# Kernel optimization log

Measured on AMD Instinct MI355X. Metric: run time of the kernel, lower is better.

## Reference

```python
import jax, jax.numpy as jnp
import numpy as np

B, S, D_IN, D_OUT, H = 2, 2048, 1024, 1024, 16
HD = D_OUT // H


def setup_inputs() -> dict:
    key = jax.random.key(0)
    ks = jax.random.split(key, 6)
    s = 0.02
    return {
        "X": jax.random.normal(ks[0], (B, S, D_IN), dtype=jnp.float32),
        "Wq": jax.random.normal(ks[1], (D_OUT, D_IN), dtype=jnp.float32) * s,
        "Wk": jax.random.normal(ks[2], (D_OUT, D_IN), dtype=jnp.float32) * s,
        "Wv": jax.random.normal(ks[3], (D_OUT, D_IN), dtype=jnp.float32) * s,
        "Wo": jax.random.normal(ks[4], (D_OUT, D_OUT), dtype=jnp.float32) * s,
        "bo": jax.random.normal(ks[5], (D_OUT,), dtype=jnp.float32) * s,
    }


def reference(X, Wq, Wk, Wv, Wo, bo):
    b, n, _ = X.shape
    # torch Linear: y = x @ W^T
    Q = (X @ Wq.T).reshape(b, n, H, HD).transpose(0, 2, 1, 3)  # [b,h,s,hd]
    K = (X @ Wk.T).reshape(b, n, H, HD).transpose(0, 2, 1, 3)
    V = (X @ Wv.T).reshape(b, n, H, HD).transpose(0, 2, 1, 3)
    S_ = jnp.einsum('bhqd,bhkd->bhqk', Q, K)  # [b,h,s,s]
    causal = jnp.triu(jnp.ones((n, n), dtype=bool), k=1)
    S_ = jnp.where(causal, -jnp.inf, S_)
    W = jax.nn.softmax(S_ / jnp.sqrt(jnp.float32(HD)), axis=-1)
    Z = jnp.einsum('bhqk,bhkd->bhqd', W, V)
    Z = Z.transpose(0, 2, 1, 3).reshape(b, n, D_OUT)
    return Z @ Wo.T + bo
```

## Files before the change

### kernel.cpp

```cpp
#include <hip/hip_runtime.h>
#include <stdint.h>

typedef __bf16 bf16x8 __attribute__((ext_vector_type(8)));
typedef float  f32x4  __attribute__((ext_vector_type(4)));

#define S_   2048
#define DM   1024
#define QSCALE 0.18033688011112042f

__device__ __forceinline__ unsigned short f2b(float f) {
    uint32_t u = __builtin_bit_cast(uint32_t, f);
    u += 0x7fffu + ((u >> 16) & 1u);
    return (unsigned short)(u >> 16);
}

__device__ __forceinline__ uint32_t pack2bf(float a, float b) {
    uint32_t ua = __builtin_bit_cast(uint32_t, a) + 0x8000u;
    uint32_t ub = __builtin_bit_cast(uint32_t, b) + 0x8000u;
    return __builtin_amdgcn_perm(ub, ua, 0x07060302);
}

__device__ __forceinline__ void glds16(const void* g, void* l) {
    __builtin_amdgcn_global_load_lds(
        (const __attribute__((address_space(1))) void*)g,
        (__attribute__((address_space(3))) void*)l, 16, 0, 0);
}

__global__ void cvt_all(const float* __restrict__ X,
                        const float* __restrict__ Wq, const float* __restrict__ Wk,
                        const float* __restrict__ Wv,
                        unsigned short* __restrict__ Xb, unsigned short* __restrict__ Wb)
{
    size_t i = ((size_t)blockIdx.x * 256 + threadIdx.x) * 4;
    const float* src;
    unsigned short* dst;
    size_t off;
    if (i < (size_t)4194304) { src = X; dst = Xb; off = i; }
    else {
        size_t j = i - 4194304;
        int sel = (int)(j >> 20);
        off = j & 1048575;
        src = (sel == 0) ? Wq : (sel == 1) ? Wk : Wv;
        dst = Wb + (size_t)sel * 1048576;
    }
    float4 v = *(const float4*)&src[off];
    uint2 o;
    o.x = pack2bf(v.x, v.y);
    o.y = pack2bf(v.z, v.w);
    *(uint2*)&dst[off] = o;
}

__global__ __launch_bounds__(256, 2)
void qkv_gemm(const unsigned short* __restrict__ Xb,
              const unsigned short* __restrict__ Wqb,
              const unsigned short* __restrict__ Wkb,
              const unsigned short* __restrict__ Wvb,
              unsigned short* __restrict__ Qo, unsigned short* __restrict__ Ko,
              unsigned short* __restrict__ Vto)
{
    __shared__ unsigned short Ash[128 * 32];
    __shared__ unsigned short Bsh[128 * 32];

    const int t = threadIdx.x;
    const int lane = t & 63, w = t >> 6;
    const int lcol = lane & 15, quad = lane >> 4;
    const int z = blockIdx.z;
    const int rowBase = ((z == 2) ? blockIdx.x : blockIdx.y) * 128;
    const int colBase = ((z == 2) ? blockIdx.y : blockIdx.x) * 128;
    const unsigned short* aPtr = (z == 2) ? Wvb : Xb;
    const unsigned short* bPtr = (z == 0) ? Wqb : (z == 1) ? Wkb : Xb;
    const int wr = (w >> 1) * 64, wc = (w & 1) * 64;

    f32x4 acc[4][4];
    #pragma unroll
    for (int i = 0; i < 4; ++i)
        #pragma unroll
        for (int j = 0; j < 4; ++j) acc[i][j] = (f32x4){0.f,0.f,0.f,0.f};

    for (int k0 = 0; k0 < DM; k0 += 32) {
        __syncthreads();
        #pragma unroll
        for (int p = 0; p < 2; ++p) {
            int ci = p * 256 + t;
            glds16(&aPtr[(size_t)(rowBase + (ci >> 2)) * DM + k0 + (ci & 3) * 8], &Ash[ci * 8]);
        }
        #pragma unroll
        for (int p = 0; p < 2; ++p) {
            int ci = p * 256 + t;
            glds16(&bPtr[(size_t)(colBase + (ci >> 2)) * DM + k0 + (ci & 3) * 8], &Bsh[ci * 8]);
        }
        __syncthreads();
        bf16x8 af[4], bfr[4];
        #pragma unroll
        for (int i = 0; i < 4; ++i) af[i]  = *(const bf16x8*)&Ash[(wr + i*16 + lcol)*32 + quad*8];
        #pragma unroll
        for (int i = 0; i < 4; ++i) bfr[i] = *(const bf16x8*)&Bsh[(wc + i*16 + lcol)*32 + quad*8];
        #pragma unroll
        for (int i = 0; i < 4; ++i)
            #pragma unroll
            for (int j = 0; j < 4; ++j)
                acc[i][j] = __builtin_amdgcn_mfma_f32_16x16x32_bf16(af[i], bfr[j], acc[i][j], 0, 0, 0);
    }

    unsigned short* Cm = (z == 0) ? Qo : (z == 1) ? Ko : Vto;
    const int ld = (z == 2) ? (S_ * 2) : DM;
    const float sc = (z == 0) ? QSCALE : 1.0f;
    #pragma unroll
    for (int i = 0; i < 4; ++i)
        #pragma unroll
        for (int j = 0; j < 4; ++j)
            #pragma unroll
            for (int r = 0; r < 4; ++r) {
                int row = rowBase + wr + i*16 + quad*4 + r;
                int col = colBase + wc + j*16 + lcol;
                Cm[(size_t)row * ld + col] = f2b(acc[i][j][r] * sc);
            }
}

__global__ __launch_bounds__(512, 4)
void attn_kernel(const unsigned short* __restrict__ Q,
                 const unsigned short* __restrict__ K,
                 const unsigned short* __restrict__ Vt,
                 unsigned short* __restrict__ Z)
{
    __shared__ unsigned short Ks[128 * 72];
    __shared__ unsigned short Vts[64 * 136];
    __shared__ unsigned short Ps[128 * 136];

    const int t = threadIdx.x;
    const int lane = t & 63, w = t >> 6;
    const int lcol = lane & 15, quad = lane >> 4;

    const int bh = blockIdx.y;
    const int b = bh >> 4, h = bh & 15;
    const int tile = (bh < 16) ? (15 - (int)blockIdx.x) : (int)blockIdx.x;
    const int q0 = tile * 128;
    const int nchunk = tile + 1;

    const unsigned short* Qg = Q + (size_t)(b * S_ + q0) * DM + h * 64;
    const unsigned short* Kg = K + (size_t)(b * S_) * DM + h * 64;
    const unsigned short* Vg = Vt + (size_t)(h * 64) * (S_ * 2) + b * S_;

    bf16x8 qf[2];
    #pragma unroll
    for (int kd = 0; kd < 2; ++kd)
        qf[kd] = *(const bf16x8*)&Qg[(size_t)(w*16 + lcol) * DM + kd*32 + quad*8];

    bool mk[4];
    #pragma unroll
    for (int r = 0; r < 4; ++r) mk[r] = (quad*4 + r) > lcol;

    float lpart = 0.f;
    f32x4 o[4];
    #pragma unroll
    for (int nd = 0; nd < 4; ++nd) o[nd] = (f32x4){0.f,0.f,0.f,0.f};

    for (int c = 0; c < nchunk; ++c) {
        const int kc = c * 128;
        __syncthreads();
        #pragma unroll
        for (int p = 0; p < 2; ++p) {
            int ci = p * 512 + t;
            *(uint4*)&Ks[(ci >> 3) * 72 + (ci & 7) * 8] =
                *(const uint4*)&Kg[(size_t)(kc + (ci >> 3)) * DM + (ci & 7) * 8];
        }
        #pragma unroll
        for (int p = 0; p < 2; ++p) {
            int ci = p * 512 + t;
            *(uint4*)&Vts[(ci >> 4) * 136 + (ci & 15) * 8] =
                *(const uint4*)&Vg[(size_t)(ci >> 4) * (S_ * 2) + kc + (ci & 15) * 8];
        }
        __syncthreads();

        const bool diag = (c == nchunk - 1);
        const int nkmax = diag ? (w + 1) : 8;
        const int kdmax = diag ? ((w >> 1) + 1) : 4;

        #pragma unroll
        for (int nk = 0; nk < 8; ++nk) {
            if (nk < nkmax) {
                f32x4 s = (f32x4){0.f,0.f,0.f,0.f};
                bf16x8 ak0 = *(const bf16x8*)&Ks[(nk*16 + lcol)*72 + quad*8];
                s = __builtin_amdgcn_mfma_f32_16x16x32_bf16(ak0, qf[0], s, 0, 0, 0);
                bf16x8 ak1 = *(const bf16x8*)&Ks[(nk*16 + lcol)*72 + 32 + quad*8];
                s = __builtin_amdgcn_mfma_f32_16x16x32_bf16(ak1, qf[1], s, 0, 0, 0);
                float p0 = __builtin_amdgcn_exp2f(s[0]);
                float p1 = __builtin_amdgcn_exp2f(s[1]);
                float p2 = __builtin_amdgcn_exp2f(s[2]);
                float p3 = __builtin_amdgcn_exp2f(s[3]);
                if (diag && nk == w) {
                    p0 = mk[0] ? 0.f : p0;
                    p1 = mk[1] ? 0.f : p1;
                    p2 = mk[2] ? 0.f : p2;
                    p3 = mk[3] ? 0.f : p3;
                }
                lpart += (p0 + p1) + (p2 + p3);
                uint2 pk;
                pk.x = pack2bf(p0, p1);
                pk.y = pack2bf(p2, p3);
                *(uint2*)&Ps[(w*16 + lcol) * 136 + nk*16 + quad*4] = pk;
            } else if (nk < 2*kdmax) {
                *(uint2*)&Ps[(w*16 + lcol) * 136 + nk*16 + quad*4] = (uint2){0u, 0u};
            }
        }

        #pragma unroll
        for (int kd2 = 0; kd2 < 4; ++kd2) {
            if (kd2 < kdmax) {
                bf16x8 ap = *(const bf16x8*)&Ps[(w*16 + lcol) * 136 + kd2*32 + quad*8];
                #pragma unroll
                for (int nd = 0; nd < 4; ++nd) {
                    bf16x8 bv = *(const bf16x8*)&Vts[(nd*16 + lcol) * 136 + kd2*32 + quad*8];
                    o[nd] = __builtin_amdgcn_mfma_f32_16x16x32_bf16(ap, bv, o[nd], 0, 0, 0);
                }
            }
        }
    }

    lpart += __shfl_xor(lpart, 16);
    lpart += __shfl_xor(lpart, 32);
    float linv = 1.0f / lpart;
    #pragma unroll
    for (int r = 0; r < 4; ++r) {
        float lr = __shfl(linv, quad*4 + r);
        unsigned short* Zr = Z + (size_t)(b*S_ + q0 + w*16 + quad*4 + r) * DM + h*64;
        #pragma unroll
        for (int nd = 0; nd < 4; ++nd)
            Zr[nd*16 + lcol] = f2b(o[nd][r] * lr);
    }
}

__global__ __launch_bounds__(512, 2)
void out_gemm(const unsigned short* __restrict__ A,
              const float* __restrict__ Wo, const float* __restrict__ bo,
              float* __restrict__ Out)
{
    __shared__ unsigned short Ash[128 * 32];
    __shared__ unsigned short Bsh[128 * 32];

    const int t = threadIdx.x;
    const int lane = t & 63, w = t >> 6;
    const int lcol = lane & 15, quad = lane >> 4;
    const int rowBase = blockIdx.y * 128;
    const int colBase = blockIdx.x * 128;
    const int wr = (w >> 2) * 64, wc = (w & 3) * 32;

    f32x4 acc[4][2];
    #pragma unroll
    for (int i = 0; i < 4; ++i)
        #pragma unroll
        for (int j = 0; j < 2; ++j) acc[i][j] = (f32x4){0.f,0.f,0.f,0.f};

    for (int k0 = 0; k0 < DM; k0 += 32) {
        __syncthreads();
        glds16(&A[(size_t)(rowBase + (t >> 2)) * DM + k0 + (t & 3) * 8], &Ash[t * 8]);
        {
            const float* sb = Wo + (size_t)(colBase + (t >> 2)) * DM + k0 + (t & 3) * 8;
            float4 v0 = ((const float4*)sb)[0];
            float4 v1 = ((const float4*)sb)[1];
            uint4 tb;
            tb.x = pack2bf(v0.x, v0.y);
            tb.y = pack2bf(v0.z, v0.w);
            tb.z = pack2bf(v1.x, v1.y);
            tb.w = pack2bf(v1.z, v1.w);
            *(uint4*)&Bsh[(t >> 2) * 32 + (t & 3) * 8] = tb;
        }
        __syncthreads();
        bf16x8 af[4], bfr[2];
        #pragma unroll
        for (int i = 0; i < 4; ++i) af[i]  = *(const bf16x8*)&Ash[(wr + i*16 + lcol)*32 + quad*8];
        #pragma unroll
        for (int j = 0; j < 2; ++j) bfr[j] = *(const bf16x8*)&Bsh[(wc + j*16 + lcol)*32 + quad*8];
        #pragma unroll
        for (int i = 0; i < 4; ++i)
            #pragma unroll
            for (int j = 0; j < 2; ++j)
                acc[i][j] = __builtin_amdgcn_mfma_f32_16x16x32_bf16(af[i], bfr[j], acc[i][j], 0, 0, 0);
    }

    float bb[2];
    #pragma unroll
    for (int j = 0; j < 2; ++j) bb[j] = bo[colBase + wc + j*16 + lcol];

    #pragma unroll
    for (int i = 0; i < 4; ++i)
        #pragma unroll
        for (int j = 0; j < 2; ++j)
            #pragma unroll
            for (int r = 0; r < 4; ++r) {
                int row = rowBase + wr + i*16 + quad*4 + r;
                int col = colBase + wc + j*16 + lcol;
                Out[(size_t)row * DM + col] = acc[i][j][r] + bb[j];
            }
}

extern "C" void kernel_launch(void* const* d_in, const int* in_sizes, int n_in,
                              void* d_out, int out_size, void* d_ws, size_t ws_size,
                              hipStream_t stream) {
    const float* X  = (const float*)d_in[0];
    const float* Wq = (const float*)d_in[1];
    const float* Wk = (const float*)d_in[2];
    const float* Wv = (const float*)d_in[3];
    const float* Wo = (const float*)d_in[4];
    const float* bo = (const float*)d_in[5];
    float* out = (float*)d_out;

    unsigned short* Xb  = (unsigned short*)d_ws;
    unsigned short* Qw  = Xb + (size_t)4096 * 1024;
    unsigned short* Kw  = Qw + (size_t)4096 * 1024;
    unsigned short* Vtw = Kw + (size_t)4096 * 1024;
    unsigned short* Zb  = Xb;
    unsigned short* Wb  = (unsigned short*)d_out;

    cvt_all<<<dim3(7168), 256, 0, stream>>>(X, Wq, Wk, Wv, Xb, Wb);
    qkv_gemm<<<dim3(8, 32, 3), 256, 0, stream>>>(Xb, Wb, Wb + (size_t)1048576,
                                                 Wb + (size_t)2097152, Qw, Kw, Vtw);
    attn_kernel<<<dim3(16, 32), 512, 0, stream>>>(Qw, Kw, Vtw, Zb);
    out_gemm<<<dim3(8, 32), 512, 0, stream>>>(Zb, Wo, bo, out);
}
```

Measured before the change: 198.2 us.

## Prefetch K/V into registers, remap attention grid per XCD, pre-convert Wo to bf16

```diff
diff --git a/kernel.cpp b/kernel.cpp
--- a/kernel.cpp
+++ b/kernel.cpp
@@ -50,6 +50,16 @@
     *(uint2*)&dst[off] = o;
 }
 
+__global__ void cvt_wo(const float* __restrict__ Wo, unsigned short* __restrict__ Wob)
+{
+    size_t i = ((size_t)blockIdx.x * 256 + threadIdx.x) * 4;
+    float4 v = *(const float4*)&Wo[i];
+    uint2 o;
+    o.x = pack2bf(v.x, v.y);
+    o.y = pack2bf(v.z, v.w);
+    *(uint2*)&Wob[i] = o;
+}
+
 __global__ __launch_bounds__(256, 2)
 void qkv_gemm(const unsigned short* __restrict__ Xb,
               const unsigned short* __restrict__ Wqb,
@@ -131,9 +141,12 @@
     const int lane = t & 63, w = t >> 6;
     const int lcol = lane & 15, quad = lane >> 4;
 
-    const int bh = blockIdx.y;
+    const int g = blockIdx.x;
+    const int xcd = g & 7, slot = g >> 3;
+    const int bh = xcd * 4 + (slot & 3);
+    const int raw = slot >> 2;
+    const int tile = (raw < 8) ? (15 - 2 * raw) : (2 * (raw - 8));
     const int b = bh >> 4, h = bh & 15;
-    const int tile = (bh < 16) ? (15 - (int)blockIdx.x) : (int)blockIdx.x;
     const int q0 = tile * 128;
     const int nchunk = tile + 1;
 
@@ -155,20 +168,27 @@
     #pragma unroll
     for (int nd = 0; nd < 4; ++nd) o[nd] = (f32x4){0.f,0.f,0.f,0.f};
 
+    const int kr = t >> 3, kch = t & 7;
+    const int vr = t >> 4, vch = t & 15;
+
+    uint4 kreg[2], vreg[2];
+    kreg[0] = *(const uint4*)&Kg[(size_t)(kr)      * DM + kch * 8];
+    kreg[1] = *(const uint4*)&Kg[(size_t)(64 + kr) * DM + kch * 8];
+    vreg[0] = *(const uint4*)&Vg[(size_t)(vr)      * (S_ * 2) + vch * 8];
+    vreg[1] = *(const uint4*)&Vg[(size_t)(32 + vr) * (S_ * 2) + vch * 8];
+
     for (int c = 0; c < nchunk; ++c) {
-        const int kc = c * 128;
-        __syncthreads();
-        #pragma unroll
-        for (int p = 0; p < 2; ++p) {
-            int ci = p * 512 + t;
-            *(uint4*)&Ks[(ci >> 3) * 72 + (ci & 7) * 8] =
-                *(const uint4*)&Kg[(size_t)(kc + (ci >> 3)) * DM + (ci & 7) * 8];
-        }
-        #pragma unroll
-        for (int p = 0; p < 2; ++p) {
-            int ci = p * 512 + t;
-            *(uint4*)&Vts[(ci >> 4) * 136 + (ci & 15) * 8] =
-                *(const uint4*)&Vg[(size_t)(ci >> 4) * (S_ * 2) + kc + (ci & 15) * 8];
+        __syncthreads();
+        *(uint4*)&Ks[(kr)      * 72 + kch * 8] = kreg[0];
+        *(uint4*)&Ks[(64 + kr) * 72 + kch * 8] = kreg[1];
+        *(uint4*)&Vts[(vr)      * 136 + vch * 8] = vreg[0];
+        *(uint4*)&Vts[(32 + vr) * 136 + vch * 8] = vreg[1];
+        if (c + 1 < nchunk) {
+            const int kn = (c + 1) * 128;
+            kreg[0] = *(const uint4*)&Kg[(size_t)(kn + kr)      * DM + kch * 8];
+            kreg[1] = *(const uint4*)&Kg[(size_t)(kn + 64 + kr) * DM + kch * 8];
+            vreg[0] = *(const uint4*)&Vg[(size_t)(vr)      * (S_ * 2) + kn + vch * 8];
+            vreg[1] = *(const uint4*)&Vg[(size_t)(32 + vr) * (S_ * 2) + kn + vch * 8];
         }
         __syncthreads();
 
@@ -232,7 +252,7 @@
 
 __global__ __launch_bounds__(512, 2)
 void out_gemm(const unsigned short* __restrict__ A,
-              const float* __restrict__ Wo, const float* __restrict__ bo,
+              const unsigned short* __restrict__ Wob, const float* __restrict__ bo,
               float* __restrict__ Out)
 {
     __shared__ unsigned short Ash[128 * 32];
@@ -254,17 +274,7 @@
     for (int k0 = 0; k0 < DM; k0 += 32) {
         __syncthreads();
         glds16(&A[(size_t)(rowBase + (t >> 2)) * DM + k0 + (t & 3) * 8], &Ash[t * 8]);
-        {
-            const float* sb = Wo + (size_t)(colBase + (t >> 2)) * DM + k0 + (t & 3) * 8;
-            float4 v0 = ((const float4*)sb)[0];
-            float4 v1 = ((const float4*)sb)[1];
-            uint4 tb;
-            tb.x = pack2bf(v0.x, v0.y);
-            tb.y = pack2bf(v0.z, v0.w);
-            tb.z = pack2bf(v1.x, v1.y);
-            tb.w = pack2bf(v1.z, v1.w);
-            *(uint4*)&Bsh[(t >> 2) * 32 + (t & 3) * 8] = tb;
-        }
+        glds16(&Wob[(size_t)(colBase + (t >> 2)) * DM + k0 + (t & 3) * 8], &Bsh[t * 8]);
         __syncthreads();
         bf16x8 af[4], bfr[2];
         #pragma unroll
@@ -310,11 +320,13 @@
     unsigned short* Kw  = Qw + (size_t)4096 * 1024;
     unsigned short* Vtw = Kw + (size_t)4096 * 1024;
     unsigned short* Zb  = Xb;
+    unsigned short* Wob = Qw;
     unsigned short* Wb  = (unsigned short*)d_out;
 
     cvt_all<<<dim3(7168), 256, 0, stream>>>(X, Wq, Wk, Wv, Xb, Wb);
     qkv_gemm<<<dim3(8, 32, 3), 256, 0, stream>>>(Xb, Wb, Wb + (size_t)1048576,
                                                  Wb + (size_t)2097152, Qw, Kw, Vtw);
-    attn_kernel<<<dim3(16, 32), 512, 0, stream>>>(Qw, Kw, Vtw, Zb);
-    out_gemm<<<dim3(8, 32), 512, 0, stream>>>(Zb, Wo, bo, out);
-}
+    attn_kernel<<<dim3(512), 512, 0, stream>>>(Qw, Kw, Vtw, Zb);
+    cvt_wo<<<dim3(1024), 256, 0, stream>>>(Wo, Wob);
+    out_gemm<<<dim3(8, 32), 512, 0, stream>>>(Zb, Wob, bo, out);
+}
```

Result: slower. 205.2 us (+3.5%).

## Give each attention wave two query subtiles and pre-convert Wo to bf16

Applied to the files above, without the earlier changes.

```diff
diff --git a/kernel.cpp b/kernel.cpp
--- a/kernel.cpp
+++ b/kernel.cpp
@@ -50,6 +50,16 @@
     *(uint2*)&dst[off] = o;
 }
 
+__global__ void cvt_wo(const float* __restrict__ Wo, unsigned short* __restrict__ Wob)
+{
+    size_t i = ((size_t)blockIdx.x * 256 + threadIdx.x) * 4;
+    float4 v = *(const float4*)&Wo[i];
+    uint2 o;
+    o.x = pack2bf(v.x, v.y);
+    o.y = pack2bf(v.z, v.w);
+    *(uint2*)&Wob[i] = o;
+}
+
 __global__ __launch_bounds__(256, 2)
 void qkv_gemm(const unsigned short* __restrict__ Xb,
               const unsigned short* __restrict__ Wqb,
@@ -117,7 +127,7 @@
             }
 }
 
-__global__ __launch_bounds__(512, 4)
+__global__ __launch_bounds__(256, 2)
 void attn_kernel(const unsigned short* __restrict__ Q,
                  const unsigned short* __restrict__ K,
                  const unsigned short* __restrict__ Vt,
@@ -131,9 +141,10 @@
     const int lane = t & 63, w = t >> 6;
     const int lcol = lane & 15, quad = lane >> 4;
 
-    const int bh = blockIdx.y;
+    const int bh = blockIdx.x;
     const int b = bh >> 4, h = bh & 15;
-    const int tile = (bh < 16) ? (15 - (int)blockIdx.x) : (int)blockIdx.x;
+    const int y = blockIdx.y;
+    const int tile = (y < 8) ? (15 - y) : (y - 8);
     const int q0 = tile * 128;
     const int nchunk = tile + 1;
 
@@ -141,98 +152,131 @@
     const unsigned short* Kg = K + (size_t)(b * S_) * DM + h * 64;
     const unsigned short* Vg = Vt + (size_t)(h * 64) * (S_ * 2) + b * S_;
 
-    bf16x8 qf[2];
-    #pragma unroll
-    for (int kd = 0; kd < 2; ++kd)
-        qf[kd] = *(const bf16x8*)&Qg[(size_t)(w*16 + lcol) * DM + kd*32 + quad*8];
+    bf16x8 qf[2][2];
+    #pragma unroll
+    for (int qs = 0; qs < 2; ++qs)
+        #pragma unroll
+        for (int kd = 0; kd < 2; ++kd)
+            qf[qs][kd] = *(const bf16x8*)&Qg[(size_t)(w*32 + qs*16 + lcol) * DM + kd*32 + quad*8];
 
     bool mk[4];
     #pragma unroll
     for (int r = 0; r < 4; ++r) mk[r] = (quad*4 + r) > lcol;
 
-    float lpart = 0.f;
-    f32x4 o[4];
-    #pragma unroll
-    for (int nd = 0; nd < 4; ++nd) o[nd] = (f32x4){0.f,0.f,0.f,0.f};
+    float lpart[2] = {0.f, 0.f};
+    f32x4 o[2][4];
+    #pragma unroll
+    for (int qs = 0; qs < 2; ++qs)
+        #pragma unroll
+        for (int nd = 0; nd < 4; ++nd) o[qs][nd] = (f32x4){0.f,0.f,0.f,0.f};
 
     for (int c = 0; c < nchunk; ++c) {
         const int kc = c * 128;
         __syncthreads();
         #pragma unroll
-        for (int p = 0; p < 2; ++p) {
-            int ci = p * 512 + t;
+        for (int p = 0; p < 4; ++p) {
+            int ci = p * 256 + t;
             *(uint4*)&Ks[(ci >> 3) * 72 + (ci & 7) * 8] =
                 *(const uint4*)&Kg[(size_t)(kc + (ci >> 3)) * DM + (ci & 7) * 8];
         }
         #pragma unroll
-        for (int p = 0; p < 2; ++p) {
-            int ci = p * 512 + t;
+        for (int p = 0; p < 4; ++p) {
+            int ci = p * 256 + t;
             *(uint4*)&Vts[(ci >> 4) * 136 + (ci & 15) * 8] =
                 *(const uint4*)&Vg[(size_t)(ci >> 4) * (S_ * 2) + kc + (ci & 15) * 8];
         }
         __syncthreads();
 
         const bool diag = (c == nchunk - 1);
-        const int nkmax = diag ? (w + 1) : 8;
-        const int kdmax = diag ? ((w >> 1) + 1) : 4;
+        const int nk0max = diag ? (2*w + 1) : 8;
+        const int nk1max = diag ? (2*w + 2) : 8;
+        const int kdmax  = diag ? (w + 1)   : 4;
 
         #pragma unroll
         for (int nk = 0; nk < 8; ++nk) {
-            if (nk < nkmax) {
-                f32x4 s = (f32x4){0.f,0.f,0.f,0.f};
+            if (nk < nk1max) {
                 bf16x8 ak0 = *(const bf16x8*)&Ks[(nk*16 + lcol)*72 + quad*8];
-                s = __builtin_amdgcn_mfma_f32_16x16x32_bf16(ak0, qf[0], s, 0, 0, 0);
                 bf16x8 ak1 = *(const bf16x8*)&Ks[(nk*16 + lcol)*72 + 32 + quad*8];
-                s = __builtin_amdgcn_mfma_f32_16x16x32_bf16(ak1, qf[1], s, 0, 0, 0);
-                float p0 = __builtin_amdgcn_exp2f(s[0]);
-                float p1 = __builtin_amdgcn_exp2f(s[1]);
-                float p2 = __builtin_amdgcn_exp2f(s[2]);
-                float p3 = __builtin_amdgcn_exp2f(s[3]);
-                if (diag && nk == w) {
-                    p0 = mk[0] ? 0.f : p0;
-                    p1 = mk[1] ? 0.f : p1;
-                    p2 = mk[2] ? 0.f : p2;
-                    p3 = mk[3] ? 0.f : p3;
+                {
+                    f32x4 s = (f32x4){0.f,0.f,0.f,0.f};
+                    s = __builtin_amdgcn_mfma_f32_16x16x32_bf16(ak0, qf[1][0], s, 0, 0, 0);
+                    s = __builtin_amdgcn_mfma_f32_16x16x32_bf16(ak1, qf[1][1], s, 0, 0, 0);
+                    float p0 = __builtin_amdgcn_exp2f(s[0]);
+                    float p1 = __builtin_amdgcn_exp2f(s[1]);
+                    float p2 = __builtin_amdgcn_exp2f(s[2]);
+                    float p3 = __builtin_amdgcn_exp2f(s[3]);
+                    if (diag && nk == 2*w + 1) {
+                        p0 = mk[0] ? 0.f : p0;
+                        p1 = mk[1] ? 0.f : p1;
+                        p2 = mk[2] ? 0.f : p2;
+                        p3 = mk[3] ? 0.f : p3;
+                    }
+                    lpart[1] += (p0 + p1) + (p2 + p3);
+                    uint2 pk;
+                    pk.x = pack2bf(p0, p1);
+                    pk.y = pack2bf(p2, p3);
+                    *(uint2*)&Ps[(w*32 + 16 + lcol) * 136 + nk*16 + quad*4] = pk;
                 }
-                lpart += (p0 + p1) + (p2 + p3);
-                uint2 pk;
-                pk.x = pack2bf(p0, p1);
-                pk.y = pack2bf(p2, p3);
-                *(uint2*)&Ps[(w*16 + lcol) * 136 + nk*16 + quad*4] = pk;
-            } else if (nk < 2*kdmax) {
-                *(uint2*)&Ps[(w*16 + lcol) * 136 + nk*16 + quad*4] = (uint2){0u, 0u};
+                if (nk < nk0max) {
+                    f32x4 s = (f32x4){0.f,0.f,0.f,0.f};
+                    s = __builtin_amdgcn_mfma_f32_16x16x32_bf16(ak0, qf[0][0], s, 0, 0, 0);
+                    s = __builtin_amdgcn_mfma_f32_16x16x32_bf16(ak1, qf[0][1], s, 0, 0, 0);
+                    float p0 = __builtin_amdgcn_exp2f(s[0]);
+                    float p1 = __builtin_amdgcn_exp2f(s[1]);
+                    float p2 = __builtin_amdgcn_exp2f(s[2]);
+                    float p3 = __builtin_amdgcn_exp2f(s[3]);
+                    if (diag && nk == 2*w) {
+                        p0 = mk[0] ? 0.f : p0;
+                        p1 = mk[1] ? 0.f : p1;
+                        p2 = mk[2] ? 0.f : p2;
+                        p3 = mk[3] ? 0.f : p3;
+                    }
+                    lpart[0] += (p0 + p1) + (p2 + p3);
+                    uint2 pk;
+                    pk.x = pack2bf(p0, p1);
+                    pk.y = pack2bf(p2, p3);
+                    *(uint2*)&Ps[(w*32 + lcol) * 136 + nk*16 + quad*4] = pk;
+                } else if (nk < 2*kdmax) {
+                    *(uint2*)&Ps[(w*32 + lcol) * 136 + nk*16 + quad*4] = (uint2){0u, 0u};
+                }
             }
         }
 
         #pragma unroll
         for (int kd2 = 0; kd2 < 4; ++kd2) {
             if (kd2 < kdmax) {
-                bf16x8 ap = *(const bf16x8*)&Ps[(w*16 + lcol) * 136 + kd2*32 + quad*8];
+                bf16x8 ap0 = *(const bf16x8*)&Ps[(w*32 +      lcol) * 136 + kd2*32 + quad*8];
+                bf16x8 ap1 = *(const bf16x8*)&Ps[(w*32 + 16 + lcol) * 136 + kd2*32 + quad*8];
                 #pragma unroll
                 for (int nd = 0; nd < 4; ++nd) {
                     bf16x8 bv = *(const bf16x8*)&Vts[(nd*16 + lcol) * 136 + kd2*32 + quad*8];
-                    o[nd] = __builtin_amdgcn_mfma_f32_16x16x32_bf16(ap, bv, o[nd], 0, 0, 0);
+                    o[0][nd] = __builtin_amdgcn_mfma_f32_16x16x32_bf16(ap0, bv, o[0][nd], 0, 0, 0);
+                    o[1][nd] = __builtin_amdgcn_mfma_f32_16x16x32_bf16(ap1, bv, o[1][nd], 0, 0, 0);
                 }
             }
         }
     }
 
-    lpart += __shfl_xor(lpart, 16);
-    lpart += __shfl_xor(lpart, 32);
-    float linv = 1.0f / lpart;
-    #pragma unroll
-    for (int r = 0; r < 4; ++r) {
-        float lr = __shfl(linv, quad*4 + r);
-        unsigned short* Zr = Z + (size_t)(b*S_ + q0 + w*16 + quad*4 + r) * DM + h*64;
-        #pragma unroll
-        for (int nd = 0; nd < 4; ++nd)
-            Zr[nd*16 + lcol] = f2b(o[nd][r] * lr);
+    #pragma unroll
+    for (int qs = 0; qs < 2; ++qs) {
+        float lp = lpart[qs];
+        lp += __shfl_xor(lp, 16);
+        lp += __shfl_xor(lp, 32);
+        float linv = 1.0f / lp;
+        #pragma unroll
+        for (int r = 0; r < 4; ++r) {
+            float lr = __shfl(linv, quad*4 + r);
+            unsigned short* Zr = Z + (size_t)(b*S_ + q0 + w*32 + qs*16 + quad*4 + r) * DM + h*64;
+            #pragma unroll
+            for (int nd = 0; nd < 4; ++nd)
+                Zr[nd*16 + lcol] = f2b(o[qs][nd][r] * lr);
+        }
     }
 }
 
 __global__ __launch_bounds__(512, 2)
 void out_gemm(const unsigned short* __restrict__ A,
-              const float* __restrict__ Wo, const float* __restrict__ bo,
+              const unsigned short* __restrict__ Wob, const float* __restrict__ bo,
               float* __restrict__ Out)
 {
     __shared__ unsigned short Ash[128 * 32];
@@ -254,17 +298,7 @@
     for (int k0 = 0; k0 < DM; k0 += 32) {
         __syncthreads();
         glds16(&A[(size_t)(rowBase + (t >> 2)) * DM + k0 + (t & 3) * 8], &Ash[t * 8]);
-        {
-            const float* sb = Wo + (size_t)(colBase + (t >> 2)) * DM + k0 + (t & 3) * 8;
-            float4 v0 = ((const float4*)sb)[0];
-            float4 v1 = ((const float4*)sb)[1];
-            uint4 tb;
-            tb.x = pack2bf(v0.x, v0.y);
-            tb.y = pack2bf(v0.z, v0.w);
-            tb.z = pack2bf(v1.x, v1.y);
-            tb.w = pack2bf(v1.z, v1.w);
-            *(uint4*)&Bsh[(t >> 2) * 32 + (t & 3) * 8] = tb;
-        }
+        glds16(&Wob[(size_t)(colBase + (t >> 2)) * DM + k0 + (t & 3) * 8], &Bsh[t * 8]);
         __syncthreads();
         bf16x8 af[4], bfr[2];
         #pragma unroll
@@ -310,11 +344,13 @@
     unsigned short* Kw  = Qw + (size_t)4096 * 1024;
     unsigned short* Vtw = Kw + (size_t)4096 * 1024;
     unsigned short* Zb  = Xb;
+    unsigned short* Wob = Qw;
     unsigned short* Wb  = (unsigned short*)d_out;
 
     cvt_all<<<dim3(7168), 256, 0, stream>>>(X, Wq, Wk, Wv, Xb, Wb);
     qkv_gemm<<<dim3(8, 32, 3), 256, 0, stream>>>(Xb, Wb, Wb + (size_t)1048576,
                                                  Wb + (size_t)2097152, Qw, Kw, Vtw);
-    attn_kernel<<<dim3(16, 32), 512, 0, stream>>>(Qw, Kw, Vtw, Zb);
-    out_gemm<<<dim3(8, 32), 512, 0, stream>>>(Zb, Wo, bo, out);
-}
+    attn_kernel<<<dim3(32, 16), 256, 0, stream>>>(Qw, Kw, Vtw, Zb);
+    cvt_wo<<<dim3(1024), 256, 0, stream>>>(Wo, Wob);
+    out_gemm<<<dim3(8, 32), 512, 0, stream>>>(Zb, Wob, bo, out);
+}
```

Result: no change. 196.4 us (-0.9%).
